# Optimization experiments

Measured on AMD Instinct MI355X. Metric: run time of the kernel, lower is better.

Reference implementation:

```python
import jax, jax.numpy as jnp
import numpy as np

INPUT_DIM = 64
HIDDEN_DIM = 10
OUTPUT_DIM = 5
BATCH = 4096


def setup_inputs() -> dict:
    key = jax.random.key(0)
    ks = jax.random.split(key, 11)
    s = 0.1
    return {
        "x": jax.random.normal(ks[0], (BATCH, INPUT_DIM), dtype=jnp.float32),
        # phi: Linear(1, H) -> ReLU -> Linear(H, O)
        "phi_W1": jax.random.normal(ks[1], (1, HIDDEN_DIM), dtype=jnp.float32) * s,
        "phi_b1": jax.random.normal(ks[2], (HIDDEN_DIM,), dtype=jnp.float32) * s,
        "phi_W2": jax.random.normal(ks[3], (HIDDEN_DIM, OUTPUT_DIM), dtype=jnp.float32) * s,
        "phi_b2": jax.random.normal(ks[4], (OUTPUT_DIM,), dtype=jnp.float32) * s,
        # attention: Linear(O, 1)
        "attn_W": jax.random.normal(ks[5], (OUTPUT_DIM, 1), dtype=jnp.float32) * s,
        "attn_b": jax.random.normal(ks[6], (1,), dtype=jnp.float32) * s,
        # psi: Linear(2*O, H) -> ReLU -> Linear(H, O)
        "psi_W1": jax.random.normal(ks[7], (2 * OUTPUT_DIM, HIDDEN_DIM), dtype=jnp.float32) * s,
        "psi_b1": jax.random.normal(ks[8], (HIDDEN_DIM,), dtype=jnp.float32) * s,
        "psi_W2": jax.random.normal(ks[9], (HIDDEN_DIM, OUTPUT_DIM), dtype=jnp.float32) * s,
        "psi_b2": jax.random.normal(ks[10], (OUTPUT_DIM,), dtype=jnp.float32) * s,
    }


def reference(x, phi_W1, phi_b1, phi_W2, phi_b2, attn_W, attn_b,
              psi_W1, psi_b1, psi_W2, psi_b2) -> jnp.ndarray:
    B, n = x.shape
    # phi applied per scalar feature, batched over (B, n).
    # x[:, :, None] @ phi_W1 == outer product since input dim is 1.
    h = jax.nn.relu(x[:, :, None] * phi_W1[0] + phi_b1)          # [B, n, H]
    phi_out = jnp.einsum('bnh,ho->bno', h, phi_W2) + phi_b2      # [B, n, O]
    # attention over the feature axis
    scores = jnp.einsum('bno,oa->bna', phi_out, attn_W) + attn_b  # [B, n, 1]
    weights = jax.nn.softmax(scores, axis=1)
    w = phi_out * weights                                        # [B, n, O]
    # all pairs i < j
    ii, jj = jnp.triu_indices(n, k=1)                            # [P]
    pair = jnp.concatenate([w[:, ii, :], w[:, jj, :]], axis=-1)  # [B, P, 2O]
    ph = jax.nn.relu(jnp.einsum('bpk,kh->bph', pair, psi_W1) + psi_b1)  # [B, P, H]
    psi_out = jnp.einsum('bph,ho->bpo', ph, psi_W2) + psi_b2     # [B, P, O]
    return jnp.sum(psi_out, axis=1)                              # [B, O]
```

## Files before the change

kernel.cpp:

```cpp
#include <hip/hip_runtime.h>
#include <math.h>

typedef float f2v __attribute__((ext_vector_type(2)));

#define BATCH 4096
#define NPAIRF 2016.0f

__device__ __forceinline__ f2v relu2(f2v t) {
    t.x = fmaxf(t.x, 0.0f);
    t.y = fmaxf(t.y, 0.0f);
    return t;
}

__global__ __launch_bounds__(256, 4) void akan_kernel(
    const float* __restrict__ x,
    const float* __restrict__ phi_W1, const float* __restrict__ phi_b1,
    const float* __restrict__ phi_W2, const float* __restrict__ phi_b2,
    const float* __restrict__ attn_W, const float* __restrict__ attn_b,
    const float* __restrict__ psi_W1, const float* __restrict__ psi_b1,
    const float* __restrict__ psi_W2, const float* __restrict__ psi_b2,
    float* __restrict__ out)
{
    __shared__ float4 lds4[4 * 384];
    const int lane = threadIdx.x & 63;
    const int wave = threadIdx.x >> 6;
    const int b = blockIdx.x * 4 + wave;
    const int wq = wave * 384;

    const float xv = x[b * 64 + lane];
    float phi_out[5];
    #pragma unroll
    for (int o = 0; o < 5; ++o) phi_out[o] = phi_b2[o];
    #pragma unroll
    for (int k = 0; k < 10; ++k) {
        const float h = fmaxf(fmaf(xv, phi_W1[k], phi_b1[k]), 0.0f);
        #pragma unroll
        for (int o = 0; o < 5; ++o) phi_out[o] = fmaf(h, phi_W2[k * 5 + o], phi_out[o]);
    }

    float score = attn_b[0];
    #pragma unroll
    for (int o = 0; o < 5; ++o) score = fmaf(phi_out[o], attn_W[o], score);
    const float e = __expf(score);
    float ssum = e;
    #pragma unroll
    for (int off = 32; off >= 1; off >>= 1) ssum += __shfl_xor(ssum, off);
    const float wgt = e / ssum;

    float w[5];
    #pragma unroll
    for (int o = 0; o < 5; ++o) w[o] = phi_out[o] * wgt;

    float u[10], v[10];
    #pragma unroll
    for (int hh = 0; hh < 10; ++hh) {
        float uu = psi_b1[hh];
        float vv = 0.0f;
        #pragma unroll
        for (int o = 0; o < 5; ++o) {
            uu = fmaf(w[o], psi_W1[o * 10 + hh], uu);
            vv = fmaf(w[o], psi_W1[(5 + o) * 10 + hh], vv);
        }
        u[hh] = uu; v[hh] = vv;
    }

    lds4[wq + 3 * lane + 0]       = make_float4(u[0], u[1], u[2], u[3]);
    lds4[wq + 3 * lane + 1]       = make_float4(u[4], u[5], u[6], u[7]);
    *(float2*)&lds4[wq + 3 * lane + 2] = make_float2(u[8], u[9]);
    lds4[wq + 192 + 3 * lane + 0] = make_float4(v[0], v[1], v[2], v[3]);
    lds4[wq + 192 + 3 * lane + 1] = make_float4(v[4], v[5], v[6], v[7]);
    *(float2*)&lds4[wq + 192 + 3 * lane + 2] = make_float2(v[8], v[9]);

    f2v U[5], V[5], S[5];
    #pragma unroll
    for (int j = 0; j < 5; ++j) {
        U[j] = (f2v){u[2 * j], u[2 * j + 1]};
        V[j] = (f2v){v[2 * j], v[2 * j + 1]};
        S[j] = (f2v){0.0f, 0.0f};
    }

    #pragma unroll
    for (int d = 1; d <= 31; ++d) {
        const int pl = lane + d;
        const int wr = pl >> 6;
        const int q  = wq + 192 + 3 * pl - 384 * wr;
        const float4 ra = lds4[q];
        const float4 rb = lds4[q + 1];
        const float2 rc = *(const float2*)&lds4[q + 2];
        const bool up = (wr == 0);
        const f2v R[5] = {{ra.x, ra.y}, {ra.z, ra.w}, {rb.x, rb.y}, {rb.z, rb.w}, {rc.x, rc.y}};
        #pragma unroll
        for (int j = 0; j < 5; ++j) {
            const f2v l = up ? U[j] : V[j];
            S[j] += relu2(l + R[j]);
        }
    }
    if (lane < 32) {
        const int q = wq + 192 + 3 * (lane + 32);
        const float4 ra = lds4[q];
        const float4 rb = lds4[q + 1];
        const float2 rc = *(const float2*)&lds4[q + 2];
        const f2v R[5] = {{ra.x, ra.y}, {ra.z, ra.w}, {rb.x, rb.y}, {rb.z, rb.w}, {rc.x, rc.y}};
        #pragma unroll
        for (int j = 0; j < 5; ++j) S[j] += relu2(U[j] + R[j]);
    }

    float s_[10];
    #pragma unroll
    for (int j = 0; j < 5; ++j) { s_[2 * j] = S[j].x; s_[2 * j + 1] = S[j].y; }

    float po[5];
    #pragma unroll
    for (int o = 0; o < 5; ++o) {
        float acc = 0.0f;
        #pragma unroll
        for (int hh = 0; hh < 10; ++hh)
            acc = fmaf(s_[hh], psi_W2[hh * 5 + o], acc);
        po[o] = acc;
    }
    #pragma unroll
    for (int o = 0; o < 5; ++o) {
        #pragma unroll
        for (int off = 32; off >= 1; off >>= 1)
            po[o] += __shfl_xor(po[o], off);
    }

    if (lane == 0) {
        #pragma unroll
        for (int o = 0; o < 5; ++o)
            out[b * 5 + o] = fmaf(NPAIRF, psi_b2[o], po[o]);
    }
}

extern "C" void kernel_launch(void* const* d_in, const int* in_sizes, int n_in,
                              void* d_out, int out_size, void* d_ws, size_t ws_size,
                              hipStream_t stream) {
    const float* x      = (const float*)d_in[0];
    const float* phi_W1 = (const float*)d_in[1];
    const float* phi_b1 = (const float*)d_in[2];
    const float* phi_W2 = (const float*)d_in[3];
    const float* phi_b2 = (const float*)d_in[4];
    const float* attn_W = (const float*)d_in[5];
    const float* attn_b = (const float*)d_in[6];
    const float* psi_W1 = (const float*)d_in[7];
    const float* psi_b1 = (const float*)d_in[8];
    const float* psi_W2 = (const float*)d_in[9];
    const float* psi_b2 = (const float*)d_in[10];
    float* outp = (float*)d_out;

    dim3 grid(BATCH / 4);
    dim3 block(256);
    akan_kernel<<<grid, block, 0, stream>>>(x, phi_W1, phi_b1, phi_W2, phi_b2,
                                            attn_W, attn_b, psi_W1, psi_b1,
                                            psi_W2, psi_b2, outp);
}
```

Baseline: 16.83 us.

## Split each batch row's pair loop across two waves with DPP reductions

Each batch row is now handled by two waves instead of one. Each wave computes phi and the u/v projections redundantly, then takes half of the 31 diagonal offsets of the pair loop, and the two partial sums are combined through shared memory after a block barrier. Wave-wide reductions switch from shfl_xor to DPP row-shift/broadcast adds with a readlane, and the division becomes a hardware reciprocal. Launch bounds rise to 8 blocks per CU and the grid doubles. The gain is more parallelism and a shorter dependent loop per wave, paid for with duplicated front-end work and two __syncthreads.

```diff
diff --git a/kernel.cpp b/kernel.cpp
--- a/kernel.cpp
+++ b/kernel.cpp
@@ -12,7 +12,22 @@
     return t;
 }
 
-__global__ __launch_bounds__(256, 4) void akan_kernel(
+template <int CTRL>
+__device__ __forceinline__ float dpp_add(float x) {
+    int y = __builtin_amdgcn_update_dpp(0, __builtin_bit_cast(int, x), CTRL, 0xf, 0xf, true);
+    return x + __builtin_bit_cast(float, y);
+}
+__device__ __forceinline__ float wave_sum63(float x) {
+    x = dpp_add<0x111>(x);
+    x = dpp_add<0x112>(x);
+    x = dpp_add<0x114>(x);
+    x = dpp_add<0x118>(x);
+    x = dpp_add<0x142>(x);
+    x = dpp_add<0x143>(x);
+    return x;
+}
+
+__global__ __launch_bounds__(256, 8) void akan_kernel(
     const float* __restrict__ x,
     const float* __restrict__ phi_W1, const float* __restrict__ phi_b1,
     const float* __restrict__ phi_W2, const float* __restrict__ phi_b2,
@@ -21,11 +36,14 @@
     const float* __restrict__ psi_W2, const float* __restrict__ psi_b2,
     float* __restrict__ out)
 {
-    __shared__ float4 lds4[4 * 384];
+    __shared__ __align__(16) float4 rows[2][2][64][3];
+    __shared__ float poS[2][2][8];
+
     const int lane = threadIdx.x & 63;
-    const int wave = threadIdx.x >> 6;
-    const int b = blockIdx.x * 4 + wave;
-    const int wq = wave * 384;
+    const int wv   = threadIdx.x >> 6;
+    const int s    = wv >> 1;
+    const int half = wv & 1;
+    const int b    = blockIdx.x * 2 + s;
 
     const float xv = x[b * 64 + lane];
     float phi_out[5];
@@ -42,72 +60,79 @@
     #pragma unroll
     for (int o = 0; o < 5; ++o) score = fmaf(phi_out[o], attn_W[o], score);
     const float e = __expf(score);
-    float ssum = e;
-    #pragma unroll
-    for (int off = 32; off >= 1; off >>= 1) ssum += __shfl_xor(ssum, off);
-    const float wgt = e / ssum;
+    const float t63 = wave_sum63(e);
+    const float ssum = __builtin_bit_cast(float,
+        __builtin_amdgcn_readlane(__builtin_bit_cast(int, t63), 63));
+    const float wgt = e * __builtin_amdgcn_rcpf(ssum);
 
     float w[5];
     #pragma unroll
     for (int o = 0; o < 5; ++o) w[o] = phi_out[o] * wgt;
 
-    float u[10], v[10];
+    f2v U[5], V[5];
     #pragma unroll
-    for (int hh = 0; hh < 10; ++hh) {
-        float uu = psi_b1[hh];
-        float vv = 0.0f;
+    for (int j = 0; j < 5; ++j) {
+        const int h0 = 2 * j, h1 = 2 * j + 1;
+        float u0 = psi_b1[h0], u1 = psi_b1[h1], v0 = 0.0f, v1 = 0.0f;
         #pragma unroll
         for (int o = 0; o < 5; ++o) {
-            uu = fmaf(w[o], psi_W1[o * 10 + hh], uu);
-            vv = fmaf(w[o], psi_W1[(5 + o) * 10 + hh], vv);
+            u0 = fmaf(w[o], psi_W1[o * 10 + h0], u0);
+            u1 = fmaf(w[o], psi_W1[o * 10 + h1], u1);
+            v0 = fmaf(w[o], psi_W1[(5 + o) * 10 + h0], v0);
+            v1 = fmaf(w[o], psi_W1[(5 + o) * 10 + h1], v1);
         }
-        u[hh] = uu; v[hh] = vv;
+        U[j] = (f2v){u0, u1};
+        V[j] = (f2v){v0, v1};
     }
 
-    lds4[wq + 3 * lane + 0]       = make_float4(u[0], u[1], u[2], u[3]);
-    lds4[wq + 3 * lane + 1]       = make_float4(u[4], u[5], u[6], u[7]);
-    *(float2*)&lds4[wq + 3 * lane + 2] = make_float2(u[8], u[9]);
-    lds4[wq + 192 + 3 * lane + 0] = make_float4(v[0], v[1], v[2], v[3]);
-    lds4[wq + 192 + 3 * lane + 1] = make_float4(v[4], v[5], v[6], v[7]);
-    *(float2*)&lds4[wq + 192 + 3 * lane + 2] = make_float2(v[8], v[9]);
+    if (half) {
+        rows[s][0][lane][0] = make_float4(V[0].x, V[0].y, V[1].x, V[1].y);
+        rows[s][0][lane][1] = make_float4(V[2].x, V[2].y, V[3].x, V[3].y);
+        *(float2*)&rows[s][0][lane][2] = make_float2(V[4].x, V[4].y);
+    } else {
+        rows[s][1][lane][0] = make_float4(U[0].x, U[0].y, U[1].x, U[1].y);
+        rows[s][1][lane][1] = make_float4(U[2].x, U[2].y, U[3].x, U[3].y);
+        *(float2*)&rows[s][1][lane][2] = make_float2(U[4].x, U[4].y);
+    }
+    __syncthreads();
 
-    f2v U[5], V[5], S[5];
+    f2v S[5];
     #pragma unroll
-    for (int j = 0; j < 5; ++j) {
-        U[j] = (f2v){u[2 * j], u[2 * j + 1]};
-        V[j] = (f2v){v[2 * j], v[2 * j + 1]};
-        S[j] = (f2v){0.0f, 0.0f};
-    }
+    for (int j = 0; j < 5; ++j) S[j] = (f2v){0.0f, 0.0f};
 
-    #pragma unroll
-    for (int d = 1; d <= 31; ++d) {
+    const int dlo   = half ? 16 : 1;
+    const int niter = half ? 16 : 15;
+    #pragma unroll 4
+    for (int t = 0; t < niter; ++t) {
+        const int d  = dlo + t;
         const int pl = lane + d;
         const int wr = pl >> 6;
-        const int q  = wq + 192 + 3 * pl - 384 * wr;
-        const float4 ra = lds4[q];
-        const float4 rb = lds4[q + 1];
-        const float2 rc = *(const float2*)&lds4[q + 2];
-        const bool up = (wr == 0);
+        const int m  = pl & 63;
+        const float4* rp = rows[s][wr][m];
+        const float4 ra = rp[0];
+        const float4 rb = rp[1];
+        const float2 rc = *(const float2*)(rp + 2);
+        const bool uplocal = (wr == 0);
         const f2v R[5] = {{ra.x, ra.y}, {ra.z, ra.w}, {rb.x, rb.y}, {rb.z, rb.w}, {rc.x, rc.y}};
         #pragma unroll
         for (int j = 0; j < 5; ++j) {
-            const f2v l = up ? U[j] : V[j];
-            S[j] += relu2(l + R[j]);
+            const f2v L = uplocal ? U[j] : V[j];
+            S[j] += relu2(L + R[j]);
         }
     }
-    if (lane < 32) {
-        const int q = wq + 192 + 3 * (lane + 32);
-        const float4 ra = lds4[q];
-        const float4 rb = lds4[q + 1];
-        const float2 rc = *(const float2*)&lds4[q + 2];
+    if (!half && lane < 32) {
+        const float4* rp = rows[s][0][lane + 32];
+        const float4 ra = rp[0];
+        const float4 rb = rp[1];
+        const float2 rc = *(const float2*)(rp + 2);
         const f2v R[5] = {{ra.x, ra.y}, {ra.z, ra.w}, {rb.x, rb.y}, {rb.z, rb.w}, {rc.x, rc.y}};
         #pragma unroll
         for (int j = 0; j < 5; ++j) S[j] += relu2(U[j] + R[j]);
     }
 
-    float s_[10];
+    float sv[10];
     #pragma unroll
-    for (int j = 0; j < 5; ++j) { s_[2 * j] = S[j].x; s_[2 * j + 1] = S[j].y; }
+    for (int j = 0; j < 5; ++j) { sv[2 * j] = S[j].x; sv[2 * j + 1] = S[j].y; }
 
     float po[5];
     #pragma unroll
@@ -115,20 +140,18 @@
         float acc = 0.0f;
         #pragma unroll
         for (int hh = 0; hh < 10; ++hh)
-            acc = fmaf(s_[hh], psi_W2[hh * 5 + o], acc);
-        po[o] = acc;
-    }
-    #pragma unroll
-    for (int o = 0; o < 5; ++o) {
-        #pragma unroll
-        for (int off = 32; off >= 1; off >>= 1)
-            po[o] += __shfl_xor(po[o], off);
+            acc = fmaf(sv[hh], psi_W2[hh * 5 + o], acc);
+        po[o] = wave_sum63(acc);
     }
 
-    if (lane == 0) {
-        #pragma unroll
-        for (int o = 0; o < 5; ++o)
-            out[b * 5 + o] = fmaf(NPAIRF, psi_b2[o], po[o]);
+    if (lane == 63) {
+        *(float4*)&poS[s][half][0] = make_float4(po[0], po[1], po[2], po[3]);
+        poS[s][half][4] = po[4];
+    }
+    __syncthreads();
+
+    if (!half && lane < 5) {
+        out[b * 5 + lane] = poS[s][0][lane] + poS[s][1][lane] + NPAIRF * psi_b2[lane];
     }
 }
 
@@ -148,7 +171,7 @@
     const float* psi_b2 = (const float*)d_in[10];
     float* outp = (float*)d_out;
 
-    dim3 grid(BATCH / 4);
+    dim3 grid(BATCH / 2);
     dim3 block(256);
     akan_kernel<<<grid, block, 0, stream>>>(x, phi_W1, phi_b1, phi_W2, phi_b2,
                                             attn_W, attn_b, psi_W1, psi_b1,
```

New measurement: 17.90 us. +6.4%, slower.

## Store psi hidden projections as bf16 in LDS and use DPP wave reductions

Applied to the files above, without the earlier changes.

The per-lane u/v hidden projections are packed into bf16 pairs in LDS, halving shared-memory traffic for the 31-step pair loop, and the layout is changed to a 16-byte chunk plus a separate word. The softmax and output shuffle reductions are replaced with DPP row/bcast sums read from lane 63, and the division becomes a hardware reciprocal. This trades accuracy, since the bf16 rounding of the psi inputs and the approximate rcp add error, for fewer LDS bytes and cheaper cross-lane reductions.

```diff
diff --git a/kernel.cpp b/kernel.cpp
--- a/kernel.cpp
+++ b/kernel.cpp
@@ -12,6 +12,33 @@
     return t;
 }
 
+template <int CTRL>
+__device__ __forceinline__ float dpp_add(float x) {
+    int y = __builtin_amdgcn_update_dpp(0, __builtin_bit_cast(int, x), CTRL, 0xf, 0xf, true);
+    return x + __builtin_bit_cast(float, y);
+}
+__device__ __forceinline__ float wave_sum63(float x) {
+    x = dpp_add<0x111>(x);
+    x = dpp_add<0x112>(x);
+    x = dpp_add<0x114>(x);
+    x = dpp_add<0x118>(x);
+    x = dpp_add<0x142>(x);
+    x = dpp_add<0x143>(x);
+    return x;
+}
+
+__device__ __forceinline__ unsigned pack_bf16(float a, float b) {
+    unsigned ua = __builtin_bit_cast(unsigned, a) + 0x8000u;
+    unsigned ub = __builtin_bit_cast(unsigned, b) + 0x8000u;
+    return (ua >> 16) | (ub & 0xffff0000u);
+}
+__device__ __forceinline__ f2v unpack_bf16(unsigned w) {
+    f2v r;
+    r.x = __builtin_bit_cast(float, w << 16);
+    r.y = __builtin_bit_cast(float, w & 0xffff0000u);
+    return r;
+}
+
 __global__ __launch_bounds__(256, 4) void akan_kernel(
     const float* __restrict__ x,
     const float* __restrict__ phi_W1, const float* __restrict__ phi_b1,
@@ -21,11 +48,12 @@
     const float* __restrict__ psi_W2, const float* __restrict__ psi_b2,
     float* __restrict__ out)
 {
-    __shared__ float4 lds4[4 * 384];
+    __shared__ __align__(16) unsigned lds[4 * 640];
+
     const int lane = threadIdx.x & 63;
     const int wave = threadIdx.x >> 6;
     const int b = blockIdx.x * 4 + wave;
-    const int wq = wave * 384;
+    unsigned* const lw = lds + wave * 640;
 
     const float xv = x[b * 64 + lane];
     float phi_out[5];
@@ -42,10 +70,10 @@
     #pragma unroll
     for (int o = 0; o < 5; ++o) score = fmaf(phi_out[o], attn_W[o], score);
     const float e = __expf(score);
-    float ssum = e;
-    #pragma unroll
-    for (int off = 32; off >= 1; off >>= 1) ssum += __shfl_xor(ssum, off);
-    const float wgt = e / ssum;
+    const float t63 = wave_sum63(e);
+    const float ssum = __builtin_bit_cast(float,
+        __builtin_amdgcn_readlane(__builtin_bit_cast(int, t63), 63));
+    const float wgt = e * __builtin_amdgcn_rcpf(ssum);
 
     float w[5];
     #pragma unroll
@@ -64,12 +92,17 @@
         u[hh] = uu; v[hh] = vv;
     }
 
-    lds4[wq + 3 * lane + 0]       = make_float4(u[0], u[1], u[2], u[3]);
-    lds4[wq + 3 * lane + 1]       = make_float4(u[4], u[5], u[6], u[7]);
-    *(float2*)&lds4[wq + 3 * lane + 2] = make_float2(u[8], u[9]);
-    lds4[wq + 192 + 3 * lane + 0] = make_float4(v[0], v[1], v[2], v[3]);
-    lds4[wq + 192 + 3 * lane + 1] = make_float4(v[4], v[5], v[6], v[7]);
-    *(float2*)&lds4[wq + 192 + 3 * lane + 2] = make_float2(v[8], v[9]);
+    {
+        uint4 mu, mv;
+        mu.x = pack_bf16(u[0], u[1]); mu.y = pack_bf16(u[2], u[3]);
+        mu.z = pack_bf16(u[4], u[5]); mu.w = pack_bf16(u[6], u[7]);
+        mv.x = pack_bf16(v[0], v[1]); mv.y = pack_bf16(v[2], v[3]);
+        mv.z = pack_bf16(v[4], v[5]); mv.w = pack_bf16(v[6], v[7]);
+        *(uint4*)&lw[4 * lane]       = mu;
+        lw[256 + lane]               = pack_bf16(u[8], u[9]);
+        *(uint4*)&lw[320 + 4 * lane] = mv;
+        lw[576 + lane]               = pack_bf16(v[8], v[9]);
+    }
 
     f2v U[5], V[5], S[5];
     #pragma unroll
@@ -82,32 +115,40 @@
     #pragma unroll
     for (int d = 1; d <= 31; ++d) {
         const int pl = lane + d;
-        const int wr = pl >> 6;
-        const int q  = wq + 192 + 3 * pl - 384 * wr;
-        const float4 ra = lds4[q];
-        const float4 rb = lds4[q + 1];
-        const float2 rc = *(const float2*)&lds4[q + 2];
-        const bool up = (wr == 0);
-        const f2v R[5] = {{ra.x, ra.y}, {ra.z, ra.w}, {rb.x, rb.y}, {rb.z, rb.w}, {rc.x, rc.y}};
-        #pragma unroll
-        for (int j = 0; j < 5; ++j) {
-            const f2v l = up ? U[j] : V[j];
-            S[j] += relu2(l + R[j]);
-        }
+        const int m = pl & 63;
+        const bool wrapped = pl >= 64;
+        const unsigned* rb = wrapped ? lw : (lw + 320);
+        const uint4 q = *(const uint4*)(rb + 4 * m);
+        const unsigned c = rb[256 + m];
+        const f2v R0 = unpack_bf16(q.x), R1 = unpack_bf16(q.y),
+                  R2 = unpack_bf16(q.z), R3 = unpack_bf16(q.w),
+                  R4 = unpack_bf16(c);
+        const f2v L0 = wrapped ? V[0] : U[0];
+        const f2v L1 = wrapped ? V[1] : U[1];
+        const f2v L2 = wrapped ? V[2] : U[2];
+        const f2v L3 = wrapped ? V[3] : U[3];
+        const f2v L4 = wrapped ? V[4] : U[4];
+        S[0] += relu2(L0 + R0);
+        S[1] += relu2(L1 + R1);
+        S[2] += relu2(L2 + R2);
+        S[3] += relu2(L3 + R3);
+        S[4] += relu2(L4 + R4);
     }
     if (lane < 32) {
-        const int q = wq + 192 + 3 * (lane + 32);
-        const float4 ra = lds4[q];
-        const float4 rb = lds4[q + 1];
-        const float2 rc = *(const float2*)&lds4[q + 2];
-        const f2v R[5] = {{ra.x, ra.y}, {ra.z, ra.w}, {rb.x, rb.y}, {rb.z, rb.w}, {rc.x, rc.y}};
-        #pragma unroll
-        for (int j = 0; j < 5; ++j) S[j] += relu2(U[j] + R[j]);
+        const int m = lane + 32;
+        const unsigned* rb = lw + 320;
+        const uint4 q = *(const uint4*)(rb + 4 * m);
+        const unsigned c = rb[256 + m];
+        S[0] += relu2(U[0] + unpack_bf16(q.x));
+        S[1] += relu2(U[1] + unpack_bf16(q.y));
+        S[2] += relu2(U[2] + unpack_bf16(q.z));
+        S[3] += relu2(U[3] + unpack_bf16(q.w));
+        S[4] += relu2(U[4] + unpack_bf16(c));
     }
 
-    float s_[10];
+    float sv[10];
     #pragma unroll
-    for (int j = 0; j < 5; ++j) { s_[2 * j] = S[j].x; s_[2 * j + 1] = S[j].y; }
+    for (int j = 0; j < 5; ++j) { sv[2 * j] = S[j].x; sv[2 * j + 1] = S[j].y; }
 
     float po[5];
     #pragma unroll
@@ -115,17 +156,11 @@
         float acc = 0.0f;
         #pragma unroll
         for (int hh = 0; hh < 10; ++hh)
-            acc = fmaf(s_[hh], psi_W2[hh * 5 + o], acc);
-        po[o] = acc;
-    }
-    #pragma unroll
-    for (int o = 0; o < 5; ++o) {
-        #pragma unroll
-        for (int off = 32; off >= 1; off >>= 1)
-            po[o] += __shfl_xor(po[o], off);
+            acc = fmaf(sv[hh], psi_W2[hh * 5 + o], acc);
+        po[o] = wave_sum63(acc);
     }
 
-    if (lane == 0) {
+    if (lane == 63) {
         #pragma unroll
         for (int o = 0; o < 5; ++o)
             out[b * 5 + o] = fmaf(NPAIRF, psi_b2[o], po[o]);
```

Result: slower. 18.98 us (+12.8%).
